# Kernel optimization log

Measured on AMD Instinct MI355X. Metric: run time of the kernel, lower is better.

Reference implementation:

```python
import jax, jax.numpy as jnp
import numpy as np

SPLINE_ORDER = 3
BN_EPS = 1e-5


def make_grid(grid_size, lo=-1.0, hi=1.0):
    # torch KANLinear grid: uniform on [lo,hi] extended by spline_order knots each side
    h = (hi - lo) / grid_size
    return jnp.arange(-SPLINE_ORDER, grid_size + SPLINE_ORDER + 1, dtype=jnp.float32) * h + lo


def b_splines(x, grid, k=SPLINE_ORDER):
    # x: [...], grid: [G+2k+1] -> bases [..., G+k] (Cox-de Boor recursion)
    x = x[..., None]
    bases = ((x >= grid[:-1]) & (x < grid[1:])).astype(x.dtype)
    for j in range(1, k + 1):
        left = (x - grid[: -(j + 1)]) / (grid[j:-1] - grid[: -(j + 1)])
        right = (grid[j + 1:] - x) / (grid[j + 1:] - grid[1:-j])
        bases = left * bases[..., :-1] + right * bases[..., 1:]
    return bases


def extract_patches(x, d):
    # 3x3 dilated sliding windows, stride 1, padding == dilation -> same HxW
    B, C, H, W = x.shape
    xp = jnp.pad(x, ((0, 0), (0, 0), (d, d), (d, d)))
    pats = [xp[:, :, ki * d:ki * d + H, kj * d:kj * d + W]
            for ki in range(3) for kj in range(3)]
    return jnp.stack(pats, axis=-1)  # [B,C,H,W,9] (kh-major, matching torch Unfold)


def batchnorm(x, g, b):
    # training-mode BN (torch default forward): batch statistics, biased variance
    mean = x.mean(axis=(0, 2, 3), keepdims=True)
    var = x.var(axis=(0, 2, 3), keepdims=True)
    return (x - mean) / jnp.sqrt(var + BN_EPS) * g[None, :, None, None] + b[None, :, None, None]


def se_block(x, w1, w2):
    y = x.mean(axis=(2, 3))                                  # [B,C]
    y = jax.nn.sigmoid(jax.nn.relu(y @ w1.T) @ w2.T)         # [B,C]
    return x * y[:, :, None, None]


def kan_conv(x, base_w, spline_w, grid, dilation):
    # one KANLinear(9->1) per (out,in) channel pair, summed over in channels
    p = extract_patches(x, dilation)                          # [B,Ci,H,W,9]
    base = jnp.einsum('bihwk,oik->bohw', jax.nn.silu(p), base_w)
    bs = b_splines(p, grid)                                   # [B,Ci,H,W,9,G+k]
    spl = jnp.einsum('bihwkg,oikg->bohw', bs, spline_w)
    return base + spl


def kan_branch(x, base_w, spline_w, grid, dilation, bn_g, bn_b, se_w1, se_w2):
    y = kan_conv(x, base_w, spline_w, grid, dilation)
    y = jax.nn.relu(batchnorm(y, bn_g, bn_b))
    return se_block(y, se_w1, se_w2)


def setup_inputs() -> dict:
    key = jax.random.key(0)
    ks = jax.random.split(key, 16)
    B, Ci, Co, H, W = 2, 64, 64, 64, 64
    r = Co // 16
    d = {"x": jax.random.normal(ks[0], (B, Ci, H, W), jnp.float32)}
    for i, (bname, G) in enumerate([(6, 3), (12, 6), (18, 9)]):
        kk = jax.random.split(ks[1 + i], 4)
        d[f"base_w{bname}"] = jax.random.normal(kk[0], (Co, Ci, 9), jnp.float32) / np.sqrt(9.0 * Ci)
        d[f"spline_w{bname}"] = jax.random.normal(kk[1], (Co, Ci, 9, G + SPLINE_ORDER), jnp.float32) * (0.1 / np.sqrt(9.0 * Ci))
        d[f"bn{bname}_g"] = jnp.ones((Co,), jnp.float32)
        d[f"bn{bname}_b"] = jnp.zeros((Co,), jnp.float32)
        d[f"se{bname}_w1"] = jax.random.normal(kk[2], (r, Co), jnp.float32) / np.sqrt(Co)
        d[f"se{bname}_w2"] = jax.random.normal(kk[3], (Co, r), jnp.float32) / np.sqrt(r)
    d["gp_conv_w"] = jax.random.normal(ks[4], (Co, Ci), jnp.float32) / np.sqrt(Ci)
    d["gp_conv_b"] = jnp.zeros((Co,), jnp.float32)
    d["gp_bn_g"] = jnp.ones((Co,), jnp.float32)
    d["gp_bn_b"] = jnp.zeros((Co,), jnp.float32)
    d["gp_se_w1"] = jax.random.normal(ks[5], (r, Co), jnp.float32) / np.sqrt(Co)
    d["gp_se_w2"] = jax.random.normal(ks[6], (Co, r), jnp.float32) / np.sqrt(r)
    d["fuse_w"] = jax.random.normal(ks[7], (Co, 4 * Co), jnp.float32) / np.sqrt(4.0 * Co)
    d["fuse_b"] = jnp.zeros((Co,), jnp.float32)
    d["fuse_bn_g"] = jnp.ones((Co,), jnp.float32)
    d["fuse_bn_b"] = jnp.zeros((Co,), jnp.float32)
    return d


def reference(x, base_w6, spline_w6, bn6_g, bn6_b, se6_w1, se6_w2,
              base_w12, spline_w12, bn12_g, bn12_b, se12_w1, se12_w2,
              base_w18, spline_w18, bn18_g, bn18_b, se18_w1, se18_w2,
              gp_conv_w, gp_conv_b, gp_bn_g, gp_bn_b, gp_se_w1, gp_se_w2,
              fuse_w, fuse_b, fuse_bn_g, fuse_bn_b):
    B, Ci, H, W = x.shape
    # global-pool branch: avgpool -> 1x1 conv -> BN -> ReLU -> SE -> bilinear
    # upsample (1x1 source => pure broadcast, align_corners irrelevant)
    gp = x.mean(axis=(2, 3)) @ gp_conv_w.T + gp_conv_b      # [B,Co]
    gp = gp[:, :, None, None]
    gp = jax.nn.relu(batchnorm(gp, gp_bn_g, gp_bn_b))
    gp = se_block(gp, gp_se_w1, gp_se_w2)
    gp = jnp.broadcast_to(gp, (B, gp.shape[1], H, W))
    # KAN dilated branches
    b6 = kan_branch(x, base_w6, spline_w6, make_grid(3), 6, bn6_g, bn6_b, se6_w1, se6_w2)
    b12 = kan_branch(x, base_w12, spline_w12, make_grid(6), 12, bn12_g, bn12_b, se12_w1, se12_w2)
    b18 = kan_branch(x, base_w18, spline_w18, make_grid(9), 18, bn18_g, bn18_b, se18_w1, se18_w2)
    cat = jnp.concatenate([b6, b12, b18, gp], axis=1)        # [B,4Co,H,W]
    out = jnp.einsum('bihw,oi->bohw', cat, fuse_w) + fuse_b[None, :, None, None]
    out = jax.nn.relu(batchnorm(out, fuse_bn_g, fuse_bn_b))
    return out
```

## Files before the change

### kernel.cpp

```cpp
#include <hip/hip_runtime.h>
#include <hip/hip_bf16.h>
#include <math.h>

#define DEV __device__ __forceinline__

static constexpr int HW  = 4096;
static constexpr int POS = 8192;
static constexpr int SLAB = 6 * 64 * 4096;

typedef __attribute__((ext_vector_type(8)))  short short8;
typedef __attribute__((ext_vector_type(16))) float floatx16;
typedef __attribute__((ext_vector_type(4)))  unsigned int uint4v;

template<int G>
DEV void bsplines(float x, float* out ) {
  const float h = 2.0f / (float)G;
  float knot[G + 7];
#pragma unroll
  for (int t = 0; t < G + 7; ++t) knot[t] = -1.0f + (float)(t - 3) * h;
  float bb[G + 6];
#pragma unroll
  for (int t = 0; t < G + 6; ++t) bb[t] = (x >= knot[t] && x < knot[t + 1]) ? 1.0f : 0.0f;
#pragma unroll
  for (int j = 1; j <= 3; ++j) {
    const float inv = (float)G / (2.0f * (float)j);
#pragma unroll
    for (int t = 0; t < G + 6 - j; ++t) {
      float left  = (x - knot[t]) * inv;
      float right = (knot[t + j + 1] - x) * inv;
      bb[t] = left * bb[t] + right * bb[t + 1];
    }
  }
#pragma unroll
  for (int t = 0; t < G + 3; ++t) out[t] = bb[t];
}

DEV float sigmoidf_(float x) { return 1.0f / (1.0f + __expf(-x)); }

DEV float block_reduce_256(float v, float* sb) {
  __syncthreads();
#pragma unroll
  for (int off = 32; off > 0; off >>= 1) v += __shfl_down(v, off, 64);
  int lane = threadIdx.x & 63, wid = threadIdx.x >> 6;
  if (lane == 0) sb[wid] = v;
  __syncthreads();
  return sb[0] + sb[1] + sb[2] + sb[3];
}


template<int CF>
DEV void wprep_body(const float* __restrict__ base_w, const float* __restrict__ spline_w,
                    __hip_bfloat16* __restrict__ Wt, int bid) {
  constexpr int KC = 64 * CF;
  int lin = bid * 256 + threadIdx.x;
  int ic = lin % KC;
  int rest = lin / KC;
  int o = rest & 63, tap = rest >> 6;
  int c = ic % CF, i = ic / CF;
  float v = (c == 0) ? base_w[(o * 64 + i) * 9 + tap]
                     : spline_w[((o * 64 + i) * 9 + tap) * (CF - 1) + (c - 1)];
  int s = ic >> 4, kk = ic & 15, q = kk >> 3, r = kk & 7, hh = o >> 5;
  int l = q * 32 + (o & 31);
  Wt[(size_t)tap * (64 * KC) + s * 1024 + hh * 512 + l * 8 + r] = __float2bfloat16(v);
}

template<int G>
DEV void c0r_body(int ki, const float* __restrict__ sw, float* __restrict__ out,
                  float* shmem ) {
  constexpr int NB = G + 3;
  int o = threadIdx.x & 63, part = threadIdx.x >> 6;
  float b0[NB];
  bsplines<G>(0.0f, b0);
  float s = 0.0f;
  for (int kj = 0; kj < 3; ++kj) {
    int tap = ki * 3 + kj;
    for (int i = part * 16; i < part * 16 + 16; ++i) {
      const float* p = sw + ((size_t)(o * 64 + i) * 9 + tap) * NB;
#pragma unroll
      for (int c = 0; c < NB; ++c) s += p[c] * b0[c];
    }
  }
  shmem[part * 64 + o] = s;
  __syncthreads();
  if (part == 0)
    out[ki * 64 + o] = shmem[o] + shmem[64 + o] + shmem[128 + o] + shmem[192 + o];
}

template<int G, int RB>
DEV void feat_stage(float xv, float s, __hip_bfloat16* lds, int ws, int i) {
  constexpr int CF = G + 4;
  constexpr int RS = 64 * CF + 16;
  float bas[G + 3];
  bsplines<G>(xv, bas);
  __hip_bfloat16* d = lds + RB + ws * RS + i * CF;
  d[0] = __float2bfloat16(s);
#pragma unroll
  for (int c = 1; c < CF; ++c) d[c] = __float2bfloat16(bas[c - 1]);
}

template<int CF, int D, int RBu>
DEV void feat_copy(__hip_bfloat16* __restrict__ F, int b, int h, int wg, const uint4v* l) {
  constexpr int WP = 64 + 2 * D;
  constexpr int KC = 64 * CF;
  uint4v* g = (uint4v*)(F + (size_t)(b * 64 + h) * WP * KC);
  for (int t = threadIdx.x; t < 32 * CF; t += 256) {
    int sc = t >> 3, r = t & 7, wl = r >> 1, k4 = r & 1;
    g[(size_t)(sc * WP + D + wg * 4 + wl) * 2 + k4] = l[RBu + wl * (8 * CF + 2) + sc * 2 + k4];
  }
}

DEV void feat_interior(const float* __restrict__ x, __hip_bfloat16* F0, __hip_bfloat16* F1,
                       __hip_bfloat16* F2, int bid, __hip_bfloat16* lds) {
  int tid = threadIdx.x;
  int ws = tid & 3, i = tid >> 2;
  int wg = bid & 15, h = (bid >> 4) & 63, b = bid >> 10;
  int w = wg * 4 + ws;
  float xv = x[((size_t)(b * 64 + i) * 64 + h) * 64 + w];
  float s = xv * sigmoidf_(xv);
  feat_stage<3, 0>(xv, s, lds, ws, i);
  feat_stage<6, 1856>(xv, s, lds, ws, i);
  feat_stage<9, 4480>(xv, s, lds, ws, i);
  __syncthreads();
  const uint4v* l = (const uint4v*)lds;
  feat_copy<7, 6, 0>(F0, b, h, wg, l);
  feat_copy<10, 12, 232>(F1, b, h, wg, l);
  feat_copy<13, 18, 560>(F2, b, h, wg, l);
}

template<int G, int D>
DEV void halo_body(__hip_bfloat16* __restrict__ F, int bidl, __hip_bfloat16* ldsb) {
  constexpr int CF = G + 4;
  constexpr int WP = 64 + 2 * D;
  constexpr int KC = 64 * CF;
  constexpr int PW = 8 * CF;
  constexpr int D2 = 2 * D;
  int tid = threadIdx.x;
  float bas0[G + 3];
  bsplines<G>(0.0f, bas0);
  for (int k = tid; k < KC; k += 256) {
    int c = k % CF;
    float v = 0.0f;
#pragma unroll
    for (int cc = 1; cc < CF; ++cc) v = (c == cc) ? bas0[cc - 1] : v;
    ldsb[k] = __float2bfloat16(v);
  }
  __syncthreads();
  const uint4v* l = (const uint4v*)ldsb;
  uint4v* g = (uint4v*)F;
#pragma unroll
  for (int u = 0; u < 16; ++u) {
    int t = bidl * 4096 + u * 256 + tid;
    int rw = t / PW, r2 = t - rw * PW;
    int sc = r2 >> 1, k4 = r2 & 1;
    int row = rw / D2, wj = rw - row * D2;
    int wp = (wj < D) ? wj : 64 + wj;
    g[(size_t)row * (WP * KC / 8) + (size_t)(sc * WP + wp) * 2 + k4] = l[sc * 2 + k4];
  }
}

__global__ void prepfeat_k(const float* __restrict__ x,
                           __hip_bfloat16* F0, __hip_bfloat16* F1, __hip_bfloat16* F2,
                           const float* bw0, const float* sw0, const float* bw1,
                           const float* sw1, const float* bw2, const float* sw2,
                           __hip_bfloat16* W0, __hip_bfloat16* W1, __hip_bfloat16* W2,
                           float* C0r, const float* fuse_w, float* fwT,
                           float* xm, float* accz ) {
  __shared__ uint4v ldsq[984];
  __shared__ float shmem[256];
  __hip_bfloat16* lds = (__hip_bfloat16*)ldsq;
  int bid = blockIdx.x, tid = threadIdx.x;
  if (bid < 2048)      { feat_interior(x, F0, F1, F2, bid, lds); return; }
  else if (bid < 2069) { halo_body<3, 6>(F0, bid - 2048, lds); return; }
  else if (bid < 2129) { halo_body<6, 12>(F1, bid - 2069, lds); return; }
  else if (bid < 2246) { halo_body<9, 18>(F2, bid - 2129, lds); return; }
  int pb = bid - 2246;
  if (pb < 1008)      { wprep_body<7>(bw0, sw0, W0, pb); }
  else if (pb < 2448) { wprep_body<10>(bw1, sw1, W1, pb - 1008); }
  else if (pb < 4320) { wprep_body<13>(bw2, sw2, W2, pb - 2448); }
  else if (pb < 4329) {
    int idx = pb - 4320, br = idx / 3, ki = idx % 3;
    if (br == 0)      c0r_body<3>(ki, sw0, C0r, shmem);
    else if (br == 1) c0r_body<6>(ki, sw1, C0r + 192, shmem);
    else              c0r_body<9>(ki, sw2, C0r + 384, shmem);
  } else if (pb < 4377) {
    int lin = (pb - 4329) * 256 + tid;
    int o = lin & 63, i2 = lin >> 6;
    fwT[i2 * 64 + o] = fuse_w[o * 256 + i2];
  } else if (pb < 4505) {
    int bi = pb - 4377;
    const float* p = x + (size_t)bi * HW;
    float s = 0.0f;
    for (int t = tid; t < HW; t += 256) s += p[t];
    s = block_reduce_256(s, shmem);
    if (tid == 0) xm[bi] = s * (1.0f / HW);
  } else {
    for (int t = tid; t < 896; t += 256) accz[t] = 0.0f;
  }
}

DEV floatx16 mfma_bf16(short8 a, short8 b, floatx16 c) {
  return __builtin_amdgcn_mfma_f32_32x32x16_bf16(a, b, c, 0, 0, 0);
}

template<int CF, int DD>
DEV void conv_dev(int ki, int b, int hp, const short* __restrict__ F,
                  const short* __restrict__ W, const float* __restrict__ C0r,
                  float* __restrict__ ypart, int br, float* __restrict__ red) {
  constexpr int KC = 64 * CF;
  constexpr int WP = 64 + 2 * DD;
  int wid = threadIdx.x >> 6;
  int wv  = wid & 1;
  int kjw = wid >> 1;
  int lane = threadIdx.x & 63;
  int lr = lane & 31, lq = lane >> 5;
  int hs = hp * 2 + wv;
  int h_out = hs - (ki - 1) * DD;
  bool valid = (h_out >= 0 && h_out < 64);
  int h_tgt = valid ? h_out : (h_out < 0 ? h_out + 64 : h_out - 64);
  float* yb = ypart + (size_t)ki * SLAB + ((size_t)((br * 2 + b) * 64 + h_tgt)) * 4096;

  floatx16 acc[2][2];
#pragma unroll
  for (int ot = 0; ot < 2; ++ot)
#pragma unroll
    for (int wh = 0; wh < 2; ++wh)
#pragma unroll
      for (int r = 0; r < 16; ++r) acc[ot][wh][r] = 0.0f;

  if (valid) {
    const short* wl_ = W + (size_t)(ki * 3 + kjw) * (64 * KC) + lane * 8;
    const short* fB  = F + (size_t)(b * 64 + hs) * WP * KC
                         + (kjw * DD + lr) * 16 + lq * 8;
#pragma unroll 4
    for (int s = 0; s < 4 * CF; ++s) {
      short8 a0 = *(const short8*)(wl_ + s * 1024);
      short8 a1 = *(const short8*)(wl_ + s * 1024 + 512);
      short8 b0 = *(const short8*)(fB + s * (WP * 16));
      short8 b1 = *(const short8*)(fB + s * (WP * 16) + 512);
      acc[0][0] = mfma_bf16(a0, b0, acc[0][0]);
      acc[0][1] = mfma_bf16(a0, b1, acc[0][1]);
      acc[1][0] = mfma_bf16(a1, b0, acc[1][0]);
      acc[1][1] = mfma_bf16(a1, b1, acc[1][1]);
    }
  }

  float* slot = red + (size_t)wv * (64 * 65) + lane * 65;
  if (kjw == 2 && valid) {
#pragma unroll
    for (int ot = 0; ot < 2; ++ot)
#pragma unroll
      for (int wh = 0; wh < 2; ++wh)
#pragma unroll
        for (int r = 0; r < 16; ++r) slot[(ot * 2 + wh) * 16 + r] = acc[ot][wh][r];
  }
  __syncthreads();
  if (kjw == 1 && valid) {
#pragma unroll
    for (int ot = 0; ot < 2; ++ot)
#pragma unroll
      for (int wh = 0; wh < 2; ++wh)
#pragma unroll
        for (int r = 0; r < 16; ++r) {
          int idx = (ot * 2 + wh) * 16 + r;
          slot[idx] += acc[ot][wh][r];
        }
  }
  __syncthreads();
  if (kjw != 0) return;

  if (!valid) {
    const float* c0 = C0r + (br * 3 + ki) * 64;
#pragma unroll
    for (int wh = 0; wh < 2; ++wh) {
      int w = wh * 32 + lr;
#pragma unroll
      for (int ot = 0; ot < 2; ++ot)
#pragma unroll
        for (int r = 0; r < 16; ++r) {
          int o = (r & 3) + 8 * (r >> 2) + 4 * lq + 32 * ot;
          yb[(size_t)o * 64 + w] = c0[o];
        }
    }
    return;
  }

#pragma unroll
  for (int ot = 0; ot < 2; ++ot)
#pragma unroll
    for (int wh = 0; wh < 2; ++wh) {
      int w = wh * 32 + lr;
#pragma unroll
      for (int r = 0; r < 16; ++r) {
        int o = (r & 3) + 8 * (r >> 2) + 4 * lq + 32 * ot;
        yb[(size_t)o * 64 + w] = acc[ot][wh][r] + slot[(ot * 2 + wh) * 16 + r];
      }
    }
}

__global__ __launch_bounds__(384) void conv_all_k(
    const short* __restrict__ F0, const short* __restrict__ F1, const short* __restrict__ F2,
    const short* __restrict__ W0, const short* __restrict__ W1, const short* __restrict__ W2,
    const float* __restrict__ C0r, float* __restrict__ ypart) {
  __shared__ float red[2 * 64 * 65];
  int bid = blockIdx.x;
  int e  = bid & 7;
  int t  = bid >> 3;
  int ki = t % 3;
  int m  = (t / 3) * 8 + e;
  int br = m >> 6, b = (m >> 5) & 1, hp = m & 31;
  if (br == 0)      conv_dev<7, 6>(ki, b, hp, F0, W0, C0r, ypart, 0, red);
  else if (br == 1) conv_dev<10, 12>(ki, b, hp, F1, W1, C0r, ypart, 1, red);
  else              conv_dev<13, 18>(ki, b, hp, F2, W2, C0r, ypart, 2, red);
}

__global__ void rb_k(float* __restrict__ yp, float* __restrict__ bnacc_s,
                     float* __restrict__ bnacc_q) {
  int bid = blockIdx.x;
  int bb = bid / 256, chunk = bid % 256;
  int br = bb >> 1;
  int tid = threadIdx.x;
  size_t base = (size_t)bb * 262144 + chunk * 1024 + tid * 4;
  float4 v = *(const float4*)(yp + base);
#pragma unroll
  for (int s2 = 1; s2 < 3; ++s2) {
    float4 u = *(const float4*)(yp + base + (size_t)s2 * SLAB);
    v.x += u.x; v.y += u.y; v.z += u.z; v.w += u.w;
  }
  *(float4*)(yp + base) = v;
  float s = v.x + v.y + v.z + v.w;
  float q = v.x * v.x + v.y * v.y + v.z * v.z + v.w * v.w;
  s += __shfl_down(s, 8, 16); s += __shfl_down(s, 4, 16);
  s += __shfl_down(s, 2, 16); s += __shfl_down(s, 1, 16);
  q += __shfl_down(q, 8, 16); q += __shfl_down(q, 4, 16);
  q += __shfl_down(q, 2, 16); q += __shfl_down(q, 1, 16);
  if ((tid & 15) == 0) {
    int o = (chunk * 16 + (tid >> 4)) & 63;
    atomicAdd(&bnacc_s[br * 64 + o], s);
    atomicAdd(&bnacc_q[br * 64 + o], q);
  }
}

__global__ void sesum_k(const float* __restrict__ y, const float* __restrict__ bnacc_s,
                        const float* __restrict__ bnacc_q,
                        const float* g0, const float* b0p, const float* g1, const float* b1p,
                        const float* g2, const float* b2p, float* __restrict__ se_acc) {
  int bid = blockIdx.x;
  int bb = bid >> 6, h = bid & 63;
  int br = bb >> 1;
  int tid = threadIdx.x;
  int o = tid >> 2, wq = tid & 3;
  const float* gptr = (br == 0) ? g0 : ((br == 1) ? g1 : g2);
  const float* bptr = (br == 0) ? b0p : ((br == 1) ? b1p : b2p);
  float mu = bnacc_s[br * 64 + o] * (1.0f / POS);
  float var = bnacc_q[br * 64 + o] * (1.0f / POS) - mu * mu;
  float kk = gptr[o] / sqrtf(var + 1e-5f);
  float cc = bptr[o] - mu * kk;
  const float* row = y + (size_t)bb * 262144 + (size_t)h * 4096 + o * 64 + wq * 16;
  float s = 0.0f;
#pragma unroll
  for (int j = 0; j < 4; ++j) {
    float4 v = *(const float4*)(row + j * 4);
    float a;
    a = v.x * kk + cc; s += (a > 0.0f) ? a : 0.0f;
    a = v.y * kk + cc; s += (a > 0.0f) ? a : 0.0f;
    a = v.z * kk + cc; s += (a > 0.0f) ? a : 0.0f;
    a = v.w * kk + cc; s += (a > 0.0f) ? a : 0.0f;
  }
  s += __shfl_down(s, 2, 4);
  s += __shfl_down(s, 1, 4);
  if (wq == 0) atomicAdd(&se_acc[bb * 64 + o], s);
}

__global__ void semlp_gp_k(const float* __restrict__ se_acc,
                           const float* __restrict__ bnacc_s, const float* __restrict__ bnacc_q,
                           const float* g0, const float* b0p, const float* g1, const float* b1p,
                           const float* g2, const float* b2p,
                           const float* w10, const float* w11, const float* w12,
                           const float* w20, const float* w21, const float* w22,
                           float* __restrict__ A1, float* __restrict__ A0,
                           const float* __restrict__ xm, const float* __restrict__ gw,
                           const float* __restrict__ gb, const float* __restrict__ bng,
                           const float* __restrict__ bnb, const float* __restrict__ gpw1,
                           const float* __restrict__ gpw2, const float* __restrict__ fuse_w,
                           float* __restrict__ fuse_gp) {
  __shared__ float sm[64];
  __shared__ float g0s[2][64], gp1s[2][64], gpvs[2][64];
  int tid = threadIdx.x;
  if (blockIdx.x < 6) {
    int bb = blockIdx.x, br = bb >> 1;
    const float* w1 = (br == 0) ? w10 : ((br == 1) ? w11 : w12);
    const float* w2 = (br == 0) ? w20 : ((br == 1) ? w21 : w22);
    const float* gptr = (br == 0) ? g0 : ((br == 1) ? g1 : g2);
    const float* bptr = (br == 0) ? b0p : ((br == 1) ? b1p : b2p);
    if (tid < 64) sm[tid] = se_acc[bb * 64 + tid] * (1.0f / HW);
    __syncthreads();
    if (tid < 64) {
      int o = tid;
      float z[4];
#pragma unroll
      for (int j = 0; j < 4; ++j) {
        float s = 0.0f;
        for (int c2 = 0; c2 < 64; ++c2) s += sm[c2] * w1[j * 64 + c2];
        z[j] = (s > 0.0f) ? s : 0.0f;
      }
      float t = 0.0f;
#pragma unroll
      for (int j = 0; j < 4; ++j) t += z[j] * w2[o * 4 + j];
      t = sigmoidf_(t);
      float mu = bnacc_s[br * 64 + o] * (1.0f / POS);
      float var = bnacc_q[br * 64 + o] * (1.0f / POS) - mu * mu;
      float kk = gptr[o] / sqrtf(var + 1e-5f);
      float cc = bptr[o] - mu * kk;
      A1[bb * 64 + o] = kk * t;
      A0[bb * 64 + o] = cc * t;
    }
  } else {
    int b = tid >> 6, o = tid & 63;
    float gv = gb[o];
    for (int i = 0; i < 64; ++i) gv += xm[b * 64 + i] * gw[o * 64 + i];
    g0s[b][o] = gv;
    __syncthreads();
    float mu = 0.5f * (g0s[0][o] + g0s[1][o]);
    float df = g0s[0][o] - g0s[1][o];
    float var = 0.25f * df * df;
    float v = (gv - mu) / sqrtf(var + 1e-5f) * bng[o] + bnb[o];
    v = (v > 0.0f) ? v : 0.0f;
    gp1s[b][o] = v;
    __syncthreads();
    float z[4];
#pragma unroll
    for (int j = 0; j < 4; ++j) {
      float s = 0.0f;
      for (int c2 = 0; c2 < 64; ++c2) s += gp1s[b][c2] * gpw1[j * 64 + c2];
      z[j] = (s > 0.0f) ? s : 0.0f;
    }
    float t = 0.0f;
#pragma unroll
    for (int j = 0; j < 4; ++j) t += z[j] * gpw2[o * 4 + j];
    t = sigmoidf_(t);
    gpvs[b][o] = v * t;
    __syncthreads();
    float fg = 0.0f;
    for (int c2 = 0; c2 < 64; ++c2) fg += fuse_w[o * 256 + 192 + c2] * gpvs[b][c2];
    fuse_gp[b * 64 + o] = fg;
  }
}

__global__ __launch_bounds__(256) void fuse_k(
    const float* __restrict__ y, const float* __restrict__ A1, const float* __restrict__ A0,
    const float* __restrict__ fwT, const float* __restrict__ fb, const float* __restrict__ fgp,
    float* __restrict__ tmp, float* __restrict__ fstat) {
  int bid = blockIdx.x;
  int b = bid >> 7, h = (bid >> 1) & 63, wh = bid & 1;
  int tid = threadIdx.x;
  int wg = tid & 7, og = tid >> 3;
  int w0 = wg * 4, o0 = og * 2;
  float acc[2][4] = {};
  __shared__ float As[64][32];
  __shared__ float Ws[64][64];
  for (int br = 0; br < 3; ++br) {
#pragma unroll
    for (int m = 0; m < 8; ++m) {
      int lin = tid + m * 256;
      int oc = lin >> 5, wl = lin & 31;
      float v = y[(size_t)(br * 2 + b) * 262144 + (size_t)h * 4096 + oc * 64 + wh * 32 + wl];
      float a1 = A1[(br * 2 + b) * 64 + oc], a0 = A0[(br * 2 + b) * 64 + oc];
      v = v * a1 + a0;
      As[oc][wl] = (v > 0.0f) ? v : 0.0f;
    }
#pragma unroll
    for (int m = 0; m < 16; ++m) {
      int lin = tid + m * 256;
      int oc = lin >> 6, ol = lin & 63;
      Ws[oc][ol] = fwT[(br * 64 + oc) * 64 + ol];
    }
    __syncthreads();
#pragma unroll 8
    for (int ict = 0; ict < 64; ++ict) {
      float4 a = *reinterpret_cast<const float4*>(&As[ict][w0]);
      float2 wv = *reinterpret_cast<const float2*>(&Ws[ict][o0]);
      acc[0][0] += wv.x * a.x; acc[0][1] += wv.x * a.y; acc[0][2] += wv.x * a.z; acc[0][3] += wv.x * a.w;
      acc[1][0] += wv.y * a.x; acc[1][1] += wv.y * a.y; acc[1][2] += wv.y * a.z; acc[1][3] += wv.y * a.w;
    }
    __syncthreads();
  }
  float* tp = tmp + (size_t)(b * 64 + h) * 4096 + wh * 32;
  float ps[2], pq[2];
#pragma unroll
  for (int oo = 0; oo < 2; ++oo) {
    int o = o0 + oo;
    float bias = fb[o] + fgp[b * 64 + o];
    float4 v = make_float4(acc[oo][0] + bias, acc[oo][1] + bias,
                           acc[oo][2] + bias, acc[oo][3] + bias);
    *reinterpret_cast<float4*>(&tp[o * 64 + w0]) = v;
    ps[oo] = v.x + v.y + v.z + v.w;
    pq[oo] = v.x * v.x + v.y * v.y + v.z * v.z + v.w * v.w;
  }
  __syncthreads();
#pragma unroll
  for (int oo = 0; oo < 2; ++oo) { As[o0 + oo][wg] = ps[oo]; Ws[o0 + oo][wg] = pq[oo]; }
  __syncthreads();
  if (tid < 64) {
    float s = 0.0f, q = 0.0f;
#pragma unroll
    for (int r = 0; r < 8; ++r) { s += As[tid][r]; q += Ws[tid][r]; }
    atomicAdd(&fstat[tid], s);
    atomicAdd(&fstat[64 + tid], q);
  }
}

__global__ void final_k(const float* __restrict__ tmp, const float* __restrict__ fstat,
                        const float* __restrict__ g, const float* __restrict__ bb,
                        float* __restrict__ out) {
  int lin = blockIdx.x * 256 + threadIdx.x;
  int w = lin & 63, h2 = (lin >> 6) & 63, o = (lin >> 12) & 63, b = lin >> 18;
  float v = tmp[((size_t)(b * 64 + h2) * 64 + o) * 64 + w];
  float m = fstat[o] * (1.0f / POS);
  float var = fstat[64 + o] * (1.0f / POS) - m * m;
  float kk = g[o] / sqrtf(var + 1e-5f);
  float r = (v - m) * kk + bb[o];
  out[lin] = (r > 0.0f) ? r : 0.0f;
}

extern "C" void kernel_launch(void* const* d_in, const int* in_sizes, int n_in,
                              void* d_out, int out_size, void* d_ws, size_t ws_size,
                              hipStream_t stream) {
  const float* x = (const float*)d_in[0];
  const float* base_w[3]   = {(const float*)d_in[1],  (const float*)d_in[7],  (const float*)d_in[13]};
  const float* spline_w[3] = {(const float*)d_in[2],  (const float*)d_in[8],  (const float*)d_in[14]};
  const float* bn_g[3]     = {(const float*)d_in[3],  (const float*)d_in[9],  (const float*)d_in[15]};
  const float* bn_b[3]     = {(const float*)d_in[4],  (const float*)d_in[10], (const float*)d_in[16]};
  const float* se_w1[3]    = {(const float*)d_in[5],  (const float*)d_in[11], (const float*)d_in[17]};
  const float* se_w2[3]    = {(const float*)d_in[6],  (const float*)d_in[12], (const float*)d_in[18]};
  const float* gp_conv_w = (const float*)d_in[19];
  const float* gp_conv_b = (const float*)d_in[20];
  const float* gp_bn_g   = (const float*)d_in[21];
  const float* gp_bn_b   = (const float*)d_in[22];
  const float* gp_se_w1  = (const float*)d_in[23];
  const float* gp_se_w2  = (const float*)d_in[24];
  const float* fuse_w    = (const float*)d_in[25];
  const float* fuse_b    = (const float*)d_in[26];
  const float* fuse_bn_g = (const float*)d_in[27];
  const float* fuse_bn_b = (const float*)d_in[28];
  float* out = (float*)d_out;

  char* wsp = (char*)d_ws;
  auto alloc = [&](size_t bytes) -> char* {
    char* p = wsp;
    wsp += (bytes + 255) & ~(size_t)255;
    return p;
  };
  __hip_bfloat16* F0 = (__hip_bfloat16*)alloc((size_t)2 * 64 * 76 * 448 * 2);
  __hip_bfloat16* F1 = (__hip_bfloat16*)alloc((size_t)2 * 64 * 88 * 640 * 2);
  __hip_bfloat16* F2 = (__hip_bfloat16*)alloc((size_t)2 * 64 * 100 * 832 * 2);
  __hip_bfloat16* W0 = (__hip_bfloat16*)alloc((size_t)9 * 64 * 448 * 2);
  __hip_bfloat16* W1 = (__hip_bfloat16*)alloc((size_t)9 * 64 * 640 * 2);
  __hip_bfloat16* W2 = (__hip_bfloat16*)alloc((size_t)9 * 64 * 832 * 2);
  float* C0r   = (float*)alloc((size_t)3 * 3 * 64 * 4);
  float* ypart = (float*)alloc((size_t)3 * SLAB * 4);
  float* y     = ypart;
  float* tmp   = ypart + SLAB;
  float* A1  = (float*)alloc(384 * 4);
  float* A0  = (float*)alloc(384 * 4);
  float* xm  = (float*)alloc(128 * 4);
  float* fgp = (float*)alloc(128 * 4);
  float* fwT = (float*)alloc((size_t)12288 * 4);
  float* accz = (float*)alloc(896 * 4);
  float* fstat   = accz;
  float* bnacc_s = accz + 128;
  float* bnacc_q = accz + 320;
  float* se_acc  = accz + 512;

  prepfeat_k<<<6752, 256, 0, stream>>>(x, F0, F1, F2,
                                       base_w[0], spline_w[0], base_w[1], spline_w[1],
                                       base_w[2], spline_w[2], W0, W1, W2, C0r,
                                       fuse_w, fwT, xm, accz);
  conv_all_k<<<576, 384, 0, stream>>>(
      (const short*)F0, (const short*)F1, (const short*)F2,
      (const short*)W0, (const short*)W1, (const short*)W2, C0r, ypart);
  rb_k<<<1536, 256, 0, stream>>>(ypart, bnacc_s, bnacc_q);
  sesum_k<<<384, 256, 0, stream>>>(y, bnacc_s, bnacc_q, bn_g[0], bn_b[0], bn_g[1], bn_b[1],
                                   bn_g[2], bn_b[2], se_acc);
  semlp_gp_k<<<7, 128, 0, stream>>>(se_acc, bnacc_s, bnacc_q, bn_g[0], bn_b[0], bn_g[1], bn_b[1],
                                    bn_g[2], bn_b[2], se_w1[0], se_w1[1], se_w1[2],
                                    se_w2[0], se_w2[1], se_w2[2], A1, A0,
                                    xm, gp_conv_w, gp_conv_b, gp_bn_g, gp_bn_b,
                                    gp_se_w1, gp_se_w2, fuse_w, fgp);
  fuse_k<<<256, 256, 0, stream>>>(y, A1, A0, fwT, fuse_b, fgp, tmp, fstat);
  final_k<<<2048, 256, 0, stream>>>(tmp, fstat, fuse_bn_g, fuse_bn_b, out);
}
```

Baseline: 243.1 us.

## Accumulate all kernel rows in-block and fuse BN statistics into conv

The conv kernel now loops over the three kernel rows inside each block, splitting work by half-width instead of by kernel row. This removes the three partial output slabs and the separate reduction kernel. BN sum and sum-of-squares are computed in the conv epilogue through wave shuffles and shared-memory atomics, then atomically added to the global accumulators. In exchange each block does up to three times more serial MFMA work, the grid shrinks from 576 to 384 blocks, and each B-fragment load now feeds only two MFMAs.

Result: slower. 248.3 us (+2.1%).

```diff
diff --git a/kernel.cpp b/kernel.cpp
--- a/kernel.cpp
+++ b/kernel.cpp
@@ -203,141 +203,109 @@
 }
 
 template<int CF, int DD>
-DEV void conv_dev(int ki, int b, int hp, const short* __restrict__ F,
+DEV void conv_dev(int wh, int b, int hp, const short* __restrict__ F,
                   const short* __restrict__ W, const float* __restrict__ C0r,
-                  float* __restrict__ ypart, int br, float* __restrict__ red) {
+                  float* __restrict__ y, int br,
+                  float* __restrict__ red ,
+                  float* __restrict__ sstat, float* __restrict__ qstat,
+                  float* __restrict__ bnacc_s, float* __restrict__ bnacc_q) {
   constexpr int KC = 64 * CF;
   constexpr int WP = 64 + 2 * DD;
-  int wid = threadIdx.x >> 6;
+  int tid = threadIdx.x;
+  int wid = tid >> 6;
   int wv  = wid & 1;
   int kjw = wid >> 1;
-  int lane = threadIdx.x & 63;
+  int lane = tid & 63;
   int lr = lane & 31, lq = lane >> 5;
-  int hs = hp * 2 + wv;
-  int h_out = hs - (ki - 1) * DD;
-  bool valid = (h_out >= 0 && h_out < 64);
-  int h_tgt = valid ? h_out : (h_out < 0 ? h_out + 64 : h_out - 64);
-  float* yb = ypart + (size_t)ki * SLAB + ((size_t)((br * 2 + b) * 64 + h_tgt)) * 4096;
-
-  floatx16 acc[2][2];
+  int h_out = hp * 2 + wv;
+
+  if (tid < 64) { sstat[tid] = 0.0f; qstat[tid] = 0.0f; }
+
+  floatx16 acc[2];
 #pragma unroll
   for (int ot = 0; ot < 2; ++ot)
 #pragma unroll
-    for (int wh = 0; wh < 2; ++wh)
-#pragma unroll
-      for (int r = 0; r < 16; ++r) acc[ot][wh][r] = 0.0f;
-
-  if (valid) {
-    const short* wl_ = W + (size_t)(ki * 3 + kjw) * (64 * KC) + lane * 8;
+    for (int r = 0; r < 16; ++r) acc[ot][r] = 0.0f;
+
+  const short* wbase = W + (size_t)kjw * (64 * KC) + lane * 8;
+#pragma unroll
+  for (int ki = 0; ki < 3; ++ki) {
+    int hs = h_out + (ki - 1) * DD;
+    if (hs < 0 || hs >= 64) continue;
+    const short* wl_ = wbase + (size_t)(ki * 3) * (64 * KC);
     const short* fB  = F + (size_t)(b * 64 + hs) * WP * KC
-                         + (kjw * DD + lr) * 16 + lq * 8;
+                         + (kjw * DD + wh * 32 + lr) * 16 + lq * 8;
 #pragma unroll 4
     for (int s = 0; s < 4 * CF; ++s) {
       short8 a0 = *(const short8*)(wl_ + s * 1024);
       short8 a1 = *(const short8*)(wl_ + s * 1024 + 512);
-      short8 b0 = *(const short8*)(fB + s * (WP * 16));
-      short8 b1 = *(const short8*)(fB + s * (WP * 16) + 512);
-      acc[0][0] = mfma_bf16(a0, b0, acc[0][0]);
-      acc[0][1] = mfma_bf16(a0, b1, acc[0][1]);
-      acc[1][0] = mfma_bf16(a1, b0, acc[1][0]);
-      acc[1][1] = mfma_bf16(a1, b1, acc[1][1]);
-    }
-  }
-
-  float* slot = red + (size_t)wv * (64 * 65) + lane * 65;
-  if (kjw == 2 && valid) {
+      short8 bf = *(const short8*)(fB + s * (WP * 16));
+      acc[0] = mfma_bf16(a0, bf, acc[0]);
+      acc[1] = mfma_bf16(a1, bf, acc[1]);
+    }
+  }
+
+  float* slot = red + (size_t)wv * (64 * 33) + lane * 33;
+  if (kjw == 2) {
 #pragma unroll
     for (int ot = 0; ot < 2; ++ot)
 #pragma unroll
-      for (int wh = 0; wh < 2; ++wh)
-#pragma unroll
-        for (int r = 0; r < 16; ++r) slot[(ot * 2 + wh) * 16 + r] = acc[ot][wh][r];
-  }
-  __syncthreads();
-  if (kjw == 1 && valid) {
+      for (int r = 0; r < 16; ++r) slot[ot * 16 + r] = acc[ot][r];
+  }
+  __syncthreads();
+  if (kjw == 1) {
 #pragma unroll
     for (int ot = 0; ot < 2; ++ot)
 #pragma unroll
-      for (int wh = 0; wh < 2; ++wh)
-#pragma unroll
-        for (int r = 0; r < 16; ++r) {
-          int idx = (ot * 2 + wh) * 16 + r;
-          slot[idx] += acc[ot][wh][r];
-        }
-  }
-  __syncthreads();
-  if (kjw != 0) return;
-
-  if (!valid) {
-    const float* c0 = C0r + (br * 3 + ki) * 64;
-#pragma unroll
-    for (int wh = 0; wh < 2; ++wh) {
-      int w = wh * 32 + lr;
-#pragma unroll
-      for (int ot = 0; ot < 2; ++ot)
-#pragma unroll
-        for (int r = 0; r < 16; ++r) {
-          int o = (r & 3) + 8 * (r >> 2) + 4 * lq + 32 * ot;
-          yb[(size_t)o * 64 + w] = c0[o];
-        }
-    }
-    return;
-  }
-
-#pragma unroll
-  for (int ot = 0; ot < 2; ++ot)
-#pragma unroll
-    for (int wh = 0; wh < 2; ++wh) {
-      int w = wh * 32 + lr;
+      for (int r = 0; r < 16; ++r) slot[ot * 16 + r] += acc[ot][r];
+  }
+  __syncthreads();
+  if (kjw == 0) {
+    const float* c0b = C0r + br * 3 * 64;
+    bool inv0 = (h_out - DD) < 0;
+    bool inv2 = (h_out + DD) >= 64;
+    float* yb = y + ((size_t)((br * 2 + b) * 64 + h_out)) * 4096;
+    int w = wh * 32 + lr;
+#pragma unroll
+    for (int ot = 0; ot < 2; ++ot)
 #pragma unroll
       for (int r = 0; r < 16; ++r) {
         int o = (r & 3) + 8 * (r >> 2) + 4 * lq + 32 * ot;
-        yb[(size_t)o * 64 + w] = acc[ot][wh][r] + slot[(ot * 2 + wh) * 16 + r];
+        float c0add = (inv0 ? c0b[o] : 0.0f) + (inv2 ? c0b[128 + o] : 0.0f);
+        float val = acc[ot][r] + slot[ot * 16 + r] + c0add;
+        yb[(size_t)o * 64 + w] = val;
+        float s = val, q = val * val;
+        s += __shfl_xor(s, 1);  q += __shfl_xor(q, 1);
+        s += __shfl_xor(s, 2);  q += __shfl_xor(q, 2);
+        s += __shfl_xor(s, 4);  q += __shfl_xor(q, 4);
+        s += __shfl_xor(s, 8);  q += __shfl_xor(q, 8);
+        s += __shfl_xor(s, 16); q += __shfl_xor(q, 16);
+        if (lr == 0) { atomicAdd(&sstat[o], s); atomicAdd(&qstat[o], q); }
       }
-    }
+  }
+  __syncthreads();
+  if (tid < 64) {
+    atomicAdd(&bnacc_s[br * 64 + tid], sstat[tid]);
+    atomicAdd(&bnacc_q[br * 64 + tid], qstat[tid]);
+  }
 }
 
 __global__ __launch_bounds__(384) void conv_all_k(
     const short* __restrict__ F0, const short* __restrict__ F1, const short* __restrict__ F2,
     const short* __restrict__ W0, const short* __restrict__ W1, const short* __restrict__ W2,
-    const float* __restrict__ C0r, float* __restrict__ ypart) {
-  __shared__ float red[2 * 64 * 65];
+    const float* __restrict__ C0r, float* __restrict__ y,
+    float* __restrict__ bnacc_s, float* __restrict__ bnacc_q) {
+  __shared__ float red[2 * 64 * 33];
+  __shared__ float sstat[64], qstat[64];
   int bid = blockIdx.x;
   int e  = bid & 7;
   int t  = bid >> 3;
-  int ki = t % 3;
-  int m  = (t / 3) * 8 + e;
+  int wh = t & 1;
+  int m  = (t >> 1) * 8 + e;
   int br = m >> 6, b = (m >> 5) & 1, hp = m & 31;
-  if (br == 0)      conv_dev<7, 6>(ki, b, hp, F0, W0, C0r, ypart, 0, red);
-  else if (br == 1) conv_dev<10, 12>(ki, b, hp, F1, W1, C0r, ypart, 1, red);
-  else              conv_dev<13, 18>(ki, b, hp, F2, W2, C0r, ypart, 2, red);
-}
-
-__global__ void rb_k(float* __restrict__ yp, float* __restrict__ bnacc_s,
-                     float* __restrict__ bnacc_q) {
-  int bid = blockIdx.x;
-  int bb = bid / 256, chunk = bid % 256;
-  int br = bb >> 1;
-  int tid = threadIdx.x;
-  size_t base = (size_t)bb * 262144 + chunk * 1024 + tid * 4;
-  float4 v = *(const float4*)(yp + base);
-#pragma unroll
-  for (int s2 = 1; s2 < 3; ++s2) {
-    float4 u = *(const float4*)(yp + base + (size_t)s2 * SLAB);
-    v.x += u.x; v.y += u.y; v.z += u.z; v.w += u.w;
-  }
-  *(float4*)(yp + base) = v;
-  float s = v.x + v.y + v.z + v.w;
-  float q = v.x * v.x + v.y * v.y + v.z * v.z + v.w * v.w;
-  s += __shfl_down(s, 8, 16); s += __shfl_down(s, 4, 16);
-  s += __shfl_down(s, 2, 16); s += __shfl_down(s, 1, 16);
-  q += __shfl_down(q, 8, 16); q += __shfl_down(q, 4, 16);
-  q += __shfl_down(q, 2, 16); q += __shfl_down(q, 1, 16);
-  if ((tid & 15) == 0) {
-    int o = (chunk * 16 + (tid >> 4)) & 63;
-    atomicAdd(&bnacc_s[br * 64 + o], s);
-    atomicAdd(&bnacc_q[br * 64 + o], q);
-  }
+  if (br == 0)      conv_dev<7, 6>(wh, b, hp, F0, W0, C0r, y, 0, red, sstat, qstat, bnacc_s, bnacc_q);
+  else if (br == 1) conv_dev<10, 12>(wh, b, hp, F1, W1, C0r, y, 1, red, sstat, qstat, bnacc_s, bnacc_q);
+  else              conv_dev<13, 18>(wh, b, hp, F2, W2, C0r, y, 2, red, sstat, qstat, bnacc_s, bnacc_q);
 }
 
 __global__ void sesum_k(const float* __restrict__ y, const float* __restrict__ bnacc_s,
@@ -557,7 +525,7 @@
   __hip_bfloat16* W1 = (__hip_bfloat16*)alloc((size_t)9 * 64 * 640 * 2);
   __hip_bfloat16* W2 = (__hip_bfloat16*)alloc((size_t)9 * 64 * 832 * 2);
   float* C0r   = (float*)alloc((size_t)3 * 3 * 64 * 4);
-  float* ypart = (float*)alloc((size_t)3 * SLAB * 4);
+  float* ypart = (float*)alloc((size_t)2 * SLAB * 4);
   float* y     = ypart;
   float* tmp   = ypart + SLAB;
   float* A1  = (float*)alloc(384 * 4);
@@ -575,10 +543,9 @@
                                        base_w[0], spline_w[0], base_w[1], spline_w[1],
                                        base_w[2], spline_w[2], W0, W1, W2, C0r,
                                        fuse_w, fwT, xm, accz);
-  conv_all_k<<<576, 384, 0, stream>>>(
+  conv_all_k<<<384, 384, 0, stream>>>(
       (const short*)F0, (const short*)F1, (const short*)F2,
-      (const short*)W0, (const short*)W1, (const short*)W2, C0r, ypart);
-  rb_k<<<1536, 256, 0, stream>>>(ypart, bnacc_s, bnacc_q);
+      (const short*)W0, (const short*)W1, (const short*)W2, C0r, y, bnacc_s, bnacc_q);
   sesum_k<<<384, 256, 0, stream>>>(y, bnacc_s, bnacc_q, bn_g[0], bn_b[0], bn_g[1], bn_b[1],
                                    bn_g[2], bn_b[2], se_acc);
   semlp_gp_k<<<7, 128, 0, stream>>>(se_acc, bnacc_s, bnacc_q, bn_g[0], bn_b[0], bn_g[1], bn_b[1],
```

## Fuse tail kernels into one persistent kernel with grid-wide barriers

Applied to the files above, without the earlier changes.

Merges the five post-conv kernels (slab reduce with BN stats, SE sum, SE MLP and global-pool branch, fuse GEMM, final BN+ReLU) into a single 512-block kernel. The stages are separated by atomic-counter grid barriers, with the counters zeroed in the prep kernel. This removes four kernel launches and their gaps, at the cost of spin-wait barriers. Correctness depends on all 512 blocks being co-resident, which is not guaranteed in general.

Measured after the change: 398.7 us. +64.0%, slower.

```diff
diff --git a/kernel.cpp b/kernel.cpp
--- a/kernel.cpp
+++ b/kernel.cpp
@@ -7,6 +7,7 @@
 static constexpr int HW  = 4096;
 static constexpr int POS = 8192;
 static constexpr int SLAB = 6 * 64 * 4096;
+static constexpr int TAILB = 512;
 
 typedef __attribute__((ext_vector_type(8)))  short short8;
 typedef __attribute__((ext_vector_type(16))) float floatx16;
@@ -45,6 +46,17 @@
   if (lane == 0) sb[wid] = v;
   __syncthreads();
   return sb[0] + sb[1] + sb[2] + sb[3];
+}
+
+DEV void gbar(int* bar, int nb) {
+  __syncthreads();
+  if (threadIdx.x == 0) {
+    __threadfence();
+    atomicAdd(bar, 1);
+    while (atomicAdd(bar, 0) < nb) __builtin_amdgcn_s_sleep(8);
+    __threadfence();
+  }
+  __syncthreads();
 }
 
 
@@ -194,7 +206,7 @@
     s = block_reduce_256(s, shmem);
     if (tid == 0) xm[bi] = s * (1.0f / HW);
   } else {
-    for (int t = tid; t < 896; t += 256) accz[t] = 0.0f;
+    for (int t = tid; t < 1024; t += 256) accz[t] = 0.0f;
   }
 }
 
@@ -313,79 +325,79 @@
   else              conv_dev<13, 18>(ki, b, hp, F2, W2, C0r, ypart, 2, red);
 }
 
-__global__ void rb_k(float* __restrict__ yp, float* __restrict__ bnacc_s,
-                     float* __restrict__ bnacc_q) {
-  int bid = blockIdx.x;
-  int bb = bid / 256, chunk = bid % 256;
-  int br = bb >> 1;
-  int tid = threadIdx.x;
-  size_t base = (size_t)bb * 262144 + chunk * 1024 + tid * 4;
-  float4 v = *(const float4*)(yp + base);
-#pragma unroll
-  for (int s2 = 1; s2 < 3; ++s2) {
-    float4 u = *(const float4*)(yp + base + (size_t)s2 * SLAB);
-    v.x += u.x; v.y += u.y; v.z += u.z; v.w += u.w;
-  }
-  *(float4*)(yp + base) = v;
-  float s = v.x + v.y + v.z + v.w;
-  float q = v.x * v.x + v.y * v.y + v.z * v.z + v.w * v.w;
-  s += __shfl_down(s, 8, 16); s += __shfl_down(s, 4, 16);
-  s += __shfl_down(s, 2, 16); s += __shfl_down(s, 1, 16);
-  q += __shfl_down(q, 8, 16); q += __shfl_down(q, 4, 16);
-  q += __shfl_down(q, 2, 16); q += __shfl_down(q, 1, 16);
-  if ((tid & 15) == 0) {
-    int o = (chunk * 16 + (tid >> 4)) & 63;
-    atomicAdd(&bnacc_s[br * 64 + o], s);
-    atomicAdd(&bnacc_q[br * 64 + o], q);
-  }
-}
-
-__global__ void sesum_k(const float* __restrict__ y, const float* __restrict__ bnacc_s,
-                        const float* __restrict__ bnacc_q,
-                        const float* g0, const float* b0p, const float* g1, const float* b1p,
-                        const float* g2, const float* b2p, float* __restrict__ se_acc) {
-  int bid = blockIdx.x;
-  int bb = bid >> 6, h = bid & 63;
-  int br = bb >> 1;
-  int tid = threadIdx.x;
-  int o = tid >> 2, wq = tid & 3;
-  const float* gptr = (br == 0) ? g0 : ((br == 1) ? g1 : g2);
-  const float* bptr = (br == 0) ? b0p : ((br == 1) ? b1p : b2p);
-  float mu = bnacc_s[br * 64 + o] * (1.0f / POS);
-  float var = bnacc_q[br * 64 + o] * (1.0f / POS) - mu * mu;
-  float kk = gptr[o] / sqrtf(var + 1e-5f);
-  float cc = bptr[o] - mu * kk;
-  const float* row = y + (size_t)bb * 262144 + (size_t)h * 4096 + o * 64 + wq * 16;
-  float s = 0.0f;
-#pragma unroll
-  for (int j = 0; j < 4; ++j) {
-    float4 v = *(const float4*)(row + j * 4);
-    float a;
-    a = v.x * kk + cc; s += (a > 0.0f) ? a : 0.0f;
-    a = v.y * kk + cc; s += (a > 0.0f) ? a : 0.0f;
-    a = v.z * kk + cc; s += (a > 0.0f) ? a : 0.0f;
-    a = v.w * kk + cc; s += (a > 0.0f) ? a : 0.0f;
-  }
-  s += __shfl_down(s, 2, 4);
-  s += __shfl_down(s, 1, 4);
-  if (wq == 0) atomicAdd(&se_acc[bb * 64 + o], s);
-}
-
-__global__ void semlp_gp_k(const float* __restrict__ se_acc,
-                           const float* __restrict__ bnacc_s, const float* __restrict__ bnacc_q,
-                           const float* g0, const float* b0p, const float* g1, const float* b1p,
-                           const float* g2, const float* b2p,
-                           const float* w10, const float* w11, const float* w12,
-                           const float* w20, const float* w21, const float* w22,
-                           float* __restrict__ A1, float* __restrict__ A0,
-                           const float* __restrict__ xm, const float* __restrict__ gw,
-                           const float* __restrict__ gb, const float* __restrict__ bng,
-                           const float* __restrict__ bnb, const float* __restrict__ gpw1,
-                           const float* __restrict__ gpw2, const float* __restrict__ fuse_w,
-                           float* __restrict__ fuse_gp) {
+__global__ __launch_bounds__(256) void tail_k(
+    float* __restrict__ yp, float* __restrict__ bnacc_s, float* __restrict__ bnacc_q,
+    const float* g0, const float* b0p, const float* g1, const float* b1p,
+    const float* g2, const float* b2p,
+    const float* w10, const float* w11, const float* w12,
+    const float* w20, const float* w21, const float* w22,
+    float* __restrict__ A1, float* __restrict__ A0,
+    const float* xm, const float* gw, const float* gb,
+    const float* bng, const float* bnb,
+    const float* gpw1, const float* gpw2,
+    const float* fuse_w, float* __restrict__ fgp,
+    const float* __restrict__ fwT, const float* fb,
+    float* __restrict__ tmp, float* __restrict__ fstat,
+    float* __restrict__ se_acc, int* __restrict__ bars,
+    const float* fbn_g, const float* fbn_b, float* __restrict__ out) {
+  __shared__ float As[64][32];
+  __shared__ float Ws[64][64];
   __shared__ float sm[64];
   __shared__ float g0s[2][64], gp1s[2][64], gpvs[2][64];
   int tid = threadIdx.x;
+
+  for (int u = blockIdx.x; u < 1536; u += gridDim.x) {
+    int bb = u / 256, chunk = u % 256;
+    int br = bb >> 1;
+    size_t base = (size_t)bb * 262144 + chunk * 1024 + tid * 4;
+    float4 v = *(const float4*)(yp + base);
+#pragma unroll
+    for (int s2 = 1; s2 < 3; ++s2) {
+      float4 u2 = *(const float4*)(yp + base + (size_t)s2 * SLAB);
+      v.x += u2.x; v.y += u2.y; v.z += u2.z; v.w += u2.w;
+    }
+    *(float4*)(yp + base) = v;
+    float s = v.x + v.y + v.z + v.w;
+    float q = v.x * v.x + v.y * v.y + v.z * v.z + v.w * v.w;
+    s += __shfl_down(s, 8, 16); s += __shfl_down(s, 4, 16);
+    s += __shfl_down(s, 2, 16); s += __shfl_down(s, 1, 16);
+    q += __shfl_down(q, 8, 16); q += __shfl_down(q, 4, 16);
+    q += __shfl_down(q, 2, 16); q += __shfl_down(q, 1, 16);
+    if ((tid & 15) == 0) {
+      int o = (chunk * 16 + (tid >> 4)) & 63;
+      atomicAdd(&bnacc_s[br * 64 + o], s);
+      atomicAdd(&bnacc_q[br * 64 + o], q);
+    }
+  }
+  gbar(&bars[0], TAILB);
+
+  for (int u = blockIdx.x; u < 384; u += gridDim.x) {
+    int bb = u >> 6, h = u & 63;
+    int br = bb >> 1;
+    int o = tid >> 2, wq = tid & 3;
+    const float* gptr = (br == 0) ? g0 : ((br == 1) ? g1 : g2);
+    const float* bptr = (br == 0) ? b0p : ((br == 1) ? b1p : b2p);
+    float mu = bnacc_s[br * 64 + o] * (1.0f / POS);
+    float var = bnacc_q[br * 64 + o] * (1.0f / POS) - mu * mu;
+    float kk = gptr[o] / sqrtf(var + 1e-5f);
+    float cc = bptr[o] - mu * kk;
+    const float* row = yp + (size_t)bb * 262144 + (size_t)h * 4096 + o * 64 + wq * 16;
+    float s = 0.0f;
+#pragma unroll
+    for (int j = 0; j < 4; ++j) {
+      float4 v = *(const float4*)(row + j * 4);
+      float a;
+      a = v.x * kk + cc; s += (a > 0.0f) ? a : 0.0f;
+      a = v.y * kk + cc; s += (a > 0.0f) ? a : 0.0f;
+      a = v.z * kk + cc; s += (a > 0.0f) ? a : 0.0f;
+      a = v.w * kk + cc; s += (a > 0.0f) ? a : 0.0f;
+    }
+    s += __shfl_down(s, 2, 4);
+    s += __shfl_down(s, 1, 4);
+    if (wq == 0) atomicAdd(&se_acc[bb * 64 + o], s);
+  }
+  gbar(&bars[1], TAILB);
+
   if (blockIdx.x < 6) {
     int bb = blockIdx.x, br = bb >> 1;
     const float* w1 = (br == 0) ? w10 : ((br == 1) ? w11 : w12);
@@ -414,112 +426,114 @@
       A1[bb * 64 + o] = kk * t;
       A0[bb * 64 + o] = cc * t;
     }
-  } else {
-    int b = tid >> 6, o = tid & 63;
-    float gv = gb[o];
-    for (int i = 0; i < 64; ++i) gv += xm[b * 64 + i] * gw[o * 64 + i];
-    g0s[b][o] = gv;
+  } else if (blockIdx.x == 6) {
+    int b = (tid >> 6) & 1, o = tid & 63;
+    float gv = 0.0f, v = 0.0f, t = 0.0f;
+    if (tid < 128) {
+      gv = gb[o];
+      for (int i = 0; i < 64; ++i) gv += xm[b * 64 + i] * gw[o * 64 + i];
+      g0s[b][o] = gv;
+    }
     __syncthreads();
-    float mu = 0.5f * (g0s[0][o] + g0s[1][o]);
-    float df = g0s[0][o] - g0s[1][o];
-    float var = 0.25f * df * df;
-    float v = (gv - mu) / sqrtf(var + 1e-5f) * bng[o] + bnb[o];
-    v = (v > 0.0f) ? v : 0.0f;
-    gp1s[b][o] = v;
+    if (tid < 128) {
+      float mu = 0.5f * (g0s[0][o] + g0s[1][o]);
+      float df = g0s[0][o] - g0s[1][o];
+      float var = 0.25f * df * df;
+      v = (gv - mu) / sqrtf(var + 1e-5f) * bng[o] + bnb[o];
+      v = (v > 0.0f) ? v : 0.0f;
+      gp1s[b][o] = v;
+    }
     __syncthreads();
-    float z[4];
-#pragma unroll
-    for (int j = 0; j < 4; ++j) {
-      float s = 0.0f;
-      for (int c2 = 0; c2 < 64; ++c2) s += gp1s[b][c2] * gpw1[j * 64 + c2];
-      z[j] = (s > 0.0f) ? s : 0.0f;
-    }
-    float t = 0.0f;
-#pragma unroll
-    for (int j = 0; j < 4; ++j) t += z[j] * gpw2[o * 4 + j];
-    t = sigmoidf_(t);
-    gpvs[b][o] = v * t;
+    if (tid < 128) {
+      float z[4];
+#pragma unroll
+      for (int j = 0; j < 4; ++j) {
+        float s = 0.0f;
+        for (int c2 = 0; c2 < 64; ++c2) s += gp1s[b][c2] * gpw1[j * 64 + c2];
+        z[j] = (s > 0.0f) ? s : 0.0f;
+      }
+#pragma unroll
+      for (int j = 0; j < 4; ++j) t += z[j] * gpw2[o * 4 + j];
+      t = sigmoidf_(t);
+      gpvs[b][o] = v * t;
+    }
     __syncthreads();
-    float fg = 0.0f;
-    for (int c2 = 0; c2 < 64; ++c2) fg += fuse_w[o * 256 + 192 + c2] * gpvs[b][c2];
-    fuse_gp[b * 64 + o] = fg;
-  }
-}
-
-__global__ __launch_bounds__(256) void fuse_k(
-    const float* __restrict__ y, const float* __restrict__ A1, const float* __restrict__ A0,
-    const float* __restrict__ fwT, const float* __restrict__ fb, const float* __restrict__ fgp,
-    float* __restrict__ tmp, float* __restrict__ fstat) {
-  int bid = blockIdx.x;
-  int b = bid >> 7, h = (bid >> 1) & 63, wh = bid & 1;
-  int tid = threadIdx.x;
-  int wg = tid & 7, og = tid >> 3;
-  int w0 = wg * 4, o0 = og * 2;
-  float acc[2][4] = {};
-  __shared__ float As[64][32];
-  __shared__ float Ws[64][64];
-  for (int br = 0; br < 3; ++br) {
-#pragma unroll
-    for (int m = 0; m < 8; ++m) {
-      int lin = tid + m * 256;
-      int oc = lin >> 5, wl = lin & 31;
-      float v = y[(size_t)(br * 2 + b) * 262144 + (size_t)h * 4096 + oc * 64 + wh * 32 + wl];
-      float a1 = A1[(br * 2 + b) * 64 + oc], a0 = A0[(br * 2 + b) * 64 + oc];
-      v = v * a1 + a0;
-      As[oc][wl] = (v > 0.0f) ? v : 0.0f;
-    }
-#pragma unroll
-    for (int m = 0; m < 16; ++m) {
-      int lin = tid + m * 256;
-      int oc = lin >> 6, ol = lin & 63;
-      Ws[oc][ol] = fwT[(br * 64 + oc) * 64 + ol];
+    if (tid < 128) {
+      float fg = 0.0f;
+      for (int c2 = 0; c2 < 64; ++c2) fg += fuse_w[o * 256 + 192 + c2] * gpvs[b][c2];
+      fgp[b * 64 + o] = fg;
+    }
+  }
+  gbar(&bars[2], TAILB);
+
+  if (blockIdx.x < 256) {
+    int bid = blockIdx.x;
+    int b = bid >> 7, h = (bid >> 1) & 63, wh = bid & 1;
+    int wg = tid & 7, og = tid >> 3;
+    int w0 = wg * 4, o0 = og * 2;
+    float acc[2][4] = {};
+    for (int br = 0; br < 3; ++br) {
+#pragma unroll
+      for (int m = 0; m < 8; ++m) {
+        int lin = tid + m * 256;
+        int oc = lin >> 5, wl = lin & 31;
+        float v = yp[(size_t)(br * 2 + b) * 262144 + (size_t)h * 4096 + oc * 64 + wh * 32 + wl];
+        float a1 = A1[(br * 2 + b) * 64 + oc], a0 = A0[(br * 2 + b) * 64 + oc];
+        v = v * a1 + a0;
+        As[oc][wl] = (v > 0.0f) ? v : 0.0f;
+      }
+#pragma unroll
+      for (int m = 0; m < 16; ++m) {
+        int lin = tid + m * 256;
+        int oc = lin >> 6, ol = lin & 63;
+        Ws[oc][ol] = fwT[(br * 64 + oc) * 64 + ol];
+      }
+      __syncthreads();
+#pragma unroll 8
+      for (int ict = 0; ict < 64; ++ict) {
+        float4 a = *reinterpret_cast<const float4*>(&As[ict][w0]);
+        float2 wv = *reinterpret_cast<const float2*>(&Ws[ict][o0]);
+        acc[0][0] += wv.x * a.x; acc[0][1] += wv.x * a.y; acc[0][2] += wv.x * a.z; acc[0][3] += wv.x * a.w;
+        acc[1][0] += wv.y * a.x; acc[1][1] += wv.y * a.y; acc[1][2] += wv.y * a.z; acc[1][3] += wv.y * a.w;
+      }
+      __syncthreads();
+    }
+    float* tp = tmp + (size_t)(b * 64 + h) * 4096 + wh * 32;
+    float ps[2], pq[2];
+#pragma unroll
+    for (int oo = 0; oo < 2; ++oo) {
+      int o = o0 + oo;
+      float bias = fb[o] + fgp[b * 64 + o];
+      float4 v = make_float4(acc[oo][0] + bias, acc[oo][1] + bias,
+                             acc[oo][2] + bias, acc[oo][3] + bias);
+      *reinterpret_cast<float4*>(&tp[o * 64 + w0]) = v;
+      ps[oo] = v.x + v.y + v.z + v.w;
+      pq[oo] = v.x * v.x + v.y * v.y + v.z * v.z + v.w * v.w;
     }
     __syncthreads();
-#pragma unroll 8
-    for (int ict = 0; ict < 64; ++ict) {
-      float4 a = *reinterpret_cast<const float4*>(&As[ict][w0]);
-      float2 wv = *reinterpret_cast<const float2*>(&Ws[ict][o0]);
-      acc[0][0] += wv.x * a.x; acc[0][1] += wv.x * a.y; acc[0][2] += wv.x * a.z; acc[0][3] += wv.x * a.w;
-      acc[1][0] += wv.y * a.x; acc[1][1] += wv.y * a.y; acc[1][2] += wv.y * a.z; acc[1][3] += wv.y * a.w;
-    }
+#pragma unroll
+    for (int oo = 0; oo < 2; ++oo) { As[o0 + oo][wg] = ps[oo]; Ws[o0 + oo][wg] = pq[oo]; }
     __syncthreads();
-  }
-  float* tp = tmp + (size_t)(b * 64 + h) * 4096 + wh * 32;
-  float ps[2], pq[2];
-#pragma unroll
-  for (int oo = 0; oo < 2; ++oo) {
-    int o = o0 + oo;
-    float bias = fb[o] + fgp[b * 64 + o];
-    float4 v = make_float4(acc[oo][0] + bias, acc[oo][1] + bias,
-                           acc[oo][2] + bias, acc[oo][3] + bias);
-    *reinterpret_cast<float4*>(&tp[o * 64 + w0]) = v;
-    ps[oo] = v.x + v.y + v.z + v.w;
-    pq[oo] = v.x * v.x + v.y * v.y + v.z * v.z + v.w * v.w;
-  }
-  __syncthreads();
-#pragma unroll
-  for (int oo = 0; oo < 2; ++oo) { As[o0 + oo][wg] = ps[oo]; Ws[o0 + oo][wg] = pq[oo]; }
-  __syncthreads();
-  if (tid < 64) {
-    float s = 0.0f, q = 0.0f;
-#pragma unroll
-    for (int r = 0; r < 8; ++r) { s += As[tid][r]; q += Ws[tid][r]; }
-    atomicAdd(&fstat[tid], s);
-    atomicAdd(&fstat[64 + tid], q);
-  }
-}
-
-__global__ void final_k(const float* __restrict__ tmp, const float* __restrict__ fstat,
-                        const float* __restrict__ g, const float* __restrict__ bb,
-                        float* __restrict__ out) {
-  int lin = blockIdx.x * 256 + threadIdx.x;
-  int w = lin & 63, h2 = (lin >> 6) & 63, o = (lin >> 12) & 63, b = lin >> 18;
-  float v = tmp[((size_t)(b * 64 + h2) * 64 + o) * 64 + w];
-  float m = fstat[o] * (1.0f / POS);
-  float var = fstat[64 + o] * (1.0f / POS) - m * m;
-  float kk = g[o] / sqrtf(var + 1e-5f);
-  float r = (v - m) * kk + bb[o];
-  out[lin] = (r > 0.0f) ? r : 0.0f;
+    if (tid < 64) {
+      float s = 0.0f, q = 0.0f;
+#pragma unroll
+      for (int r = 0; r < 8; ++r) { s += As[tid][r]; q += Ws[tid][r]; }
+      atomicAdd(&fstat[tid], s);
+      atomicAdd(&fstat[64 + tid], q);
+    }
+  }
+  gbar(&bars[3], TAILB);
+
+  for (int u = blockIdx.x; u < 2048; u += gridDim.x) {
+    int lin = u * 256 + tid;
+    int w = lin & 63, h2 = (lin >> 6) & 63, o = (lin >> 12) & 63, b = lin >> 18;
+    float v = tmp[((size_t)(b * 64 + h2) * 64 + o) * 64 + w];
+    float m = fstat[o] * (1.0f / POS);
+    float var = fstat[64 + o] * (1.0f / POS) - m * m;
+    float kk = fbn_g[o] / sqrtf(var + 1e-5f);
+    float r = (v - m) * kk + fbn_b[o];
+    out[lin] = (r > 0.0f) ? r : 0.0f;
+  }
 }
 
 extern "C" void kernel_launch(void* const* d_in, const int* in_sizes, int n_in,
@@ -558,18 +572,19 @@
   __hip_bfloat16* W2 = (__hip_bfloat16*)alloc((size_t)9 * 64 * 832 * 2);
   float* C0r   = (float*)alloc((size_t)3 * 3 * 64 * 4);
   float* ypart = (float*)alloc((size_t)3 * SLAB * 4);
-  float* y     = ypart;
+  float* yp    = ypart;
   float* tmp   = ypart + SLAB;
   float* A1  = (float*)alloc(384 * 4);
   float* A0  = (float*)alloc(384 * 4);
   float* xm  = (float*)alloc(128 * 4);
   float* fgp = (float*)alloc(128 * 4);
   float* fwT = (float*)alloc((size_t)12288 * 4);
-  float* accz = (float*)alloc(896 * 4);
+  float* accz = (float*)alloc(1024 * 4);
   float* fstat   = accz;
   float* bnacc_s = accz + 128;
   float* bnacc_q = accz + 320;
   float* se_acc  = accz + 512;
+  int*   bars    = (int*)(accz + 896);
 
   prepfeat_k<<<6752, 256, 0, stream>>>(x, F0, F1, F2,
                                        base_w[0], spline_w[0], base_w[1], spline_w[1],
@@ -578,14 +593,11 @@
   conv_all_k<<<576, 384, 0, stream>>>(
       (const short*)F0, (const short*)F1, (const short*)F2,
       (const short*)W0, (const short*)W1, (const short*)W2, C0r, ypart);
-  rb_k<<<1536, 256, 0, stream>>>(ypart, bnacc_s, bnacc_q);
-  sesum_k<<<384, 256, 0, stream>>>(y, bnacc_s, bnacc_q, bn_g[0], bn_b[0], bn_g[1], bn_b[1],
-                                   bn_g[2], bn_b[2], se_acc);
-  semlp_gp_k<<<7, 128, 0, stream>>>(se_acc, bnacc_s, bnacc_q, bn_g[0], bn_b[0], bn_g[1], bn_b[1],
-                                    bn_g[2], bn_b[2], se_w1[0], se_w1[1], se_w1[2],
-                                    se_w2[0], se_w2[1], se_w2[2], A1, A0,
-                                    xm, gp_conv_w, gp_conv_b, gp_bn_g, gp_bn_b,
-                                    gp_se_w1, gp_se_w2, fuse_w, fgp);
-  fuse_k<<<256, 256, 0, stream>>>(y, A1, A0, fwT, fuse_b, fgp, tmp, fstat);
-  final_k<<<2048, 256, 0, stream>>>(tmp, fstat, fuse_bn_g, fuse_bn_b, out);
-}
+  tail_k<<<TAILB, 256, 0, stream>>>(
+      yp, bnacc_s, bnacc_q,
+      bn_g[0], bn_b[0], bn_g[1], bn_b[1], bn_g[2], bn_b[2],
+      se_w1[0], se_w1[1], se_w1[2], se_w2[0], se_w2[1], se_w2[2],
+      A1, A0, xm, gp_conv_w, gp_conv_b, gp_bn_g, gp_bn_b,
+      gp_se_w1, gp_se_w2, fuse_w, fgp, fwT, fuse_b,
+      tmp, fstat, se_acc, bars, fuse_bn_g, fuse_bn_b, out);
+}
```
